# Kernel optimization log

Measured on AMD Instinct MI355X. Metric: run time of the kernel, lower is better.

## Reference

```python
import jax, jax.numpy as jnp
import numpy as np

WINDOW_SIZE = 11
SIGMA = 1.5
C1 = 0.0001
C2 = 0.0009


def _gaussian_kernel(window_size, channels):
    # 1D gaussian, sigma=1.5 (standard SSIM window), normalized
    ax = np.arange(window_size, dtype=np.float32) - (window_size - 1) / 2.0
    g = np.exp(-(ax ** 2) / (2.0 * SIGMA ** 2))
    g = g / g.sum()
    k2d = np.outer(g, g).astype(np.float32)  # [w, w], sums to 1
    # depthwise kernel, OIHW with groups=channels -> [C, 1, w, w]
    return jnp.asarray(np.tile(k2d[None, None], (channels, 1, 1, 1)))


def _dwconv(x, kernel):
    p = WINDOW_SIZE // 2
    return jax.lax.conv_general_dilated(
        x, kernel,
        window_strides=(1, 1),
        padding=[(p, p), (p, p)],
        dimension_numbers=('NCHW', 'OIHW', 'NCHW'),
        feature_group_count=x.shape[1],
    )


def setup_inputs() -> dict:
    key = jax.random.key(0)
    k1, k2 = jax.random.split(key)
    B, C, H, W = 16, 3, 512, 512
    x = jax.random.uniform(k1, (B, C, H, W), dtype=jnp.float32)
    y = jax.random.uniform(k2, (B, C, H, W), dtype=jnp.float32)
    return {"x": x, "y": y}


def reference(x, y):
    kernel = _gaussian_kernel(WINDOW_SIZE, x.shape[1])
    mean_sr = _dwconv(x, kernel)
    mean_hr = _dwconv(y, kernel)
    mean_sr_sq = mean_sr * mean_sr
    mean_hr_sq = mean_hr * mean_hr
    var_sr = _dwconv(x * x, kernel) - mean_sr_sq
    var_hr = _dwconv(y * y, kernel) - mean_hr_sq
    covar = _dwconv(x * y, kernel) - mean_sr * mean_hr
    ssim_pix = ((2.0 * mean_sr * mean_hr + C1) * (2.0 * covar + C2)
                / ((mean_sr_sq + mean_hr_sq + C1) * (var_sr + var_hr + C2)))
    ssim_mean = jnp.mean(ssim_pix)
    loss = -jnp.log10(ssim_mean)
    return (loss, ssim_mean)
```

## Files before the change

### kernel.cpp

```cpp
#include <hip/hip_runtime.h>
#include <hip/hip_fp16.h>
#include <math.h>

#define IMG    512
#define TWD    64
#define NSTRIP 2
#define BROWS  64
#define WIN    42
#define HS2    34
#define NBLK   3072
#define NPIX   12582912.0

constexpr float G[11] = {
    0.00102838f, 0.00759876f, 0.03600077f, 0.10936069f, 0.21300554f,
    0.26601173f,
    0.21300554f, 0.10936069f, 0.03600077f, 0.00759876f, 0.00102838f};

__device__ __forceinline__ void issue_loads(
    const float* __restrict__ px, const float* __restrict__ py, int gc0,
    float4 (&fx)[6], float4 (&fy)[6])
{
#pragma unroll
    for (int i = 0; i < 6; ++i) {
        int gcl = min(max(gc0 + 4 * i, 0), IMG - 4);
        fx[i] = *(const float4*)(px + gcl);
        fy[i] = *(const float4*)(py + gcl);
    }
}

__device__ __forceinline__ void conv_store(
    __half2 (&hb2)[4][WIN][HS2],
    const float4 (&fx)[6], const float4 (&fy)[6],
    int grow, int gc0, int bufrow, int hg)
{
    const float rm = ((unsigned)grow < IMG) ? 1.f : 0.f;
    float ax[8] = {}, ay[8] = {}, ass[8] = {}, axy[8] = {};
#pragma unroll
    for (int i = 0; i < 6; ++i) {
        const float gm = ((unsigned)(gc0 + 4 * i) < IMG) ? rm : 0.f;
        const float vx4[4] = {fx[i].x, fx[i].y, fx[i].z, fx[i].w};
        const float vy4[4] = {fy[i].x, fy[i].y, fy[i].z, fy[i].w};
#pragma unroll
        for (int c = 0; c < 4; ++c) {
            const int j = 4 * i + c;
            if (j < 3 || j > 20) continue;
            const float a  = vx4[c] * gm;
            const float b  = vy4[c] * gm;
            const float ss = fmaf(a, a, b * b);
            const float xy = a * b;
#pragma unroll
            for (int e = 0; e < 8; ++e) {
                const int k = j - 3 - e;
                if (k >= 0 && k <= 10) {
                    ax[e]  = fmaf(G[k], a,  ax[e]);
                    ay[e]  = fmaf(G[k], b,  ay[e]);
                    ass[e] = fmaf(G[k], ss, ass[e]);
                    axy[e] = fmaf(G[k], xy, axy[e]);
                }
            }
        }
    }
    const int p0 = 4 * hg;
#pragma unroll
    for (int p = 0; p < 4; ++p) {
        hb2[0][bufrow][p0 + p] = __floats2half2_rn(ax[2*p],  ax[2*p+1]);
        hb2[1][bufrow][p0 + p] = __floats2half2_rn(ay[2*p],  ay[2*p+1]);
        hb2[2][bufrow][p0 + p] = __floats2half2_rn(ass[2*p], ass[2*p+1]);
        hb2[3][bufrow][p0 + p] = __floats2half2_rn(axy[2*p], axy[2*p+1]);
    }
}

__device__ __forceinline__ float vpass16(
    const __half2 (&hb2)[4][WIN][HS2], const __half2 (&Gh)[11],
    int rb, int cg)
{
    __half2 vr[4][4];
    const __half2 z2 = __floats2half2_rn(0.f, 0.f);
#pragma unroll
    for (int q = 0; q < 4; ++q)
#pragma unroll
        for (int j = 0; j < 4; ++j) vr[q][j] = z2;
#pragma unroll
    for (int q = 0; q < 4; ++q)
#pragma unroll
        for (int k = 0; k < 14; ++k) {
            __half2 v = hb2[q][rb + k][cg];
#pragma unroll
            for (int j = 0; j < 4; ++j)
                if (k - j >= 0 && k - j <= 10)
                    vr[q][j] = __hfma2(Gh[k - j], v, vr[q][j]);
        }
    float s = 0.f;
#pragma unroll
    for (int j = 0; j < 4; ++j) {
        float2 mxv  = __half22float2(vr[0][j]);
        float2 myv  = __half22float2(vr[1][j]);
        float2 mssv = __half22float2(vr[2][j]);
        float2 mxyv = __half22float2(vr[3][j]);
        const float mxa[2]  = {mxv.x, mxv.y};
        const float mya[2]  = {myv.x, myv.y};
        const float mssa[2] = {mssv.x, mssv.y};
        const float mxya[2] = {mxyv.x, mxyv.y};
#pragma unroll
        for (int e = 0; e < 2; ++e) {
            float mx = mxa[e], my = mya[e];
            float mss = mssa[e], mxy = mxya[e];
            float mx2 = mx * mx, my2 = my * my, mxmy = mx * my;
            float num = (2.f * mxmy + 0.0001f) * (2.f * (mxy - mxmy) + 0.0009f);
            float den = (mx2 + my2 + 0.0001f) * ((mss - mx2 - my2) + 0.0009f);
            s += num * __builtin_amdgcn_rcpf(den);
        }
    }
    return s;
}

__global__ __launch_bounds__(256) void ssim_tile_kernel(
    const float* __restrict__ x, const float* __restrict__ y,
    float* __restrict__ partial)
{
    __shared__ __half2 hb2[4][WIN][HS2];
    __shared__ float wsum[4];

    const int tid = threadIdx.x;
    const int bx = blockIdx.x, by = blockIdx.y;
    const int c0 = bx * TWD;
    const int rbase0 = by * BROWS;
    const size_t ioff = (size_t)blockIdx.z * IMG * IMG;
    const float* __restrict__ xb = x + ioff;
    const float* __restrict__ yb = y + ioff;

    __half2 Gh[11];
#pragma unroll
    for (int k = 0; k < 11; ++k) Gh[k] = __floats2half2_rn(G[k], G[k]);

    const int hrow = tid >> 3;
    const int hg   = tid & 7;
    const int gc0  = c0 - 8 + 8 * hg;
    const int cg   = tid & 31;
    const int rb   = (tid >> 5) * 4;
    float lsum = 0.f;

    float4 pfx[6], pfy[6];

    {
        int brow = tid >> 3, g = tid & 7;
        int grow = rbase0 - 5 + brow;
        int tg0 = c0 - 8 + 8 * g;
        const float* px = xb + min(max(grow, 0), IMG - 1) * IMG;
        const float* py = yb + min(max(grow, 0), IMG - 1) * IMG;
        float4 fx[6], fy[6];
        issue_loads(px, py, tg0, fx, fy);
        conv_store(hb2, fx, fy, grow, tg0, brow, g);
    }
    if (tid < 80) {
        int t = tid + 256;
        int brow = t >> 3, g = t & 7;
        int grow = rbase0 - 5 + brow;
        int tg0 = c0 - 8 + 8 * g;
        const float* px = xb + min(max(grow, 0), IMG - 1) * IMG;
        const float* py = yb + min(max(grow, 0), IMG - 1) * IMG;
        float4 fx[6], fy[6];
        issue_loads(px, py, tg0, fx, fy);
        conv_store(hb2, fx, fy, grow, tg0, brow, g);
    }
    {
        int grow = rbase0 + 32 + 5 + hrow;
        const float* px = xb + min(max(grow, 0), IMG - 1) * IMG;
        const float* py = yb + min(max(grow, 0), IMG - 1) * IMG;
        issue_loads(px, py, gc0, pfx, pfy);
    }
    __syncthreads();
    lsum += vpass16(hb2, Gh, rb, cg);
    __syncthreads();

    for (int s = 1; s < NSTRIP; ++s) {
#pragma unroll
        for (int k = 0; k < 3; ++k) {
            int idx = tid + k * 256;
            if (idx < 640) {
                int q = idx / 160, rem = idx - q * 160;
                int rr = rem >> 4, p = rem & 15;
                *(float2*)&hb2[q][rr][2 * p] =
                    *(const float2*)&hb2[q][32 + rr][2 * p];
            }
        }
        __syncthreads();
        {
            int grow = rbase0 + 32 * s + 5 + hrow;
            conv_store(hb2, pfx, pfy, grow, gc0, 10 + hrow, hg);
        }
        if (s < NSTRIP - 1) {
            int grow = rbase0 + 32 * (s + 1) + 5 + hrow;
            const float* px = xb + min(max(grow, 0), IMG - 1) * IMG;
            const float* py = yb + min(max(grow, 0), IMG - 1) * IMG;
            issue_loads(px, py, gc0, pfx, pfy);
        }
        __syncthreads();
        lsum += vpass16(hb2, Gh, rb, cg);
        __syncthreads();
    }

#pragma unroll
    for (int off = 32; off > 0; off >>= 1)
        lsum += __shfl_down(lsum, off, 64);
    if ((tid & 63) == 0) wsum[tid >> 6] = lsum;
    __syncthreads();
    if (tid == 0) {
        float ssum = wsum[0] + wsum[1] + wsum[2] + wsum[3];
        int bid = bx + 8 * (by + 8 * blockIdx.z);
        partial[bid] = ssum;
    }
}

__global__ __launch_bounds__(1024) void ssim_reduce_kernel(
    const float* __restrict__ partial, float* __restrict__ out)
{
    __shared__ double ws[16];
    const int tid = threadIdx.x;
    double s = 0.0;
#pragma unroll
    for (int i = 0; i < NBLK / 1024; ++i) s += (double)partial[tid + i * 1024];
#pragma unroll
    for (int off = 32; off > 0; off >>= 1)
        s += __shfl_down(s, off, 64);
    if ((tid & 63) == 0) ws[tid >> 6] = s;
    __syncthreads();
    if (tid == 0) {
        double t = 0.0;
#pragma unroll
        for (int w = 0; w < 16; ++w) t += ws[w];
        double mean = t / NPIX;
        out[0] = (float)(-log10(mean));
        out[1] = (float)mean;
    }
}

extern "C" void kernel_launch(void* const* d_in, const int* in_sizes, int n_in,
                              void* d_out, int out_size, void* d_ws, size_t ws_size,
                              hipStream_t stream)
{
    const float* x = (const float*)d_in[0];
    const float* y = (const float*)d_in[1];
    float* out     = (float*)d_out;
    float* partial = (float*)d_ws;

    dim3 grid(8, 8, 48);
    ssim_tile_kernel<<<grid, 256, 0, stream>>>(x, y, partial);
    ssim_reduce_kernel<<<1, 1024, 0, stream>>>(partial, out);
}
```

Before: 52.53 us.

## Use single-strip 32-row tiles, XCD-aware block remap, unmasked interior path

Drops the two-strip sliding window with its register prefetch and LDS row shift. Each block now handles one 32-row strip, so twice as many blocks are launched and each does a full 42-row horizontal pass. Block IDs are remapped so consecutive hardware block IDs, which spread across XCDs, cover contiguous image regions. Interior tiles skip clamping and masking via a templated fast path. In exchange, halo rows are recomputed more often (42 per 32 output rows instead of 74 per 64), which adds global load and horizontal-pass work.

```diff
diff --git a/kernel.cpp b/kernel.cpp
--- a/kernel.cpp
+++ b/kernel.cpp
@@ -2,50 +2,46 @@
 #include <hip/hip_fp16.h>
 #include <math.h>
 
-#define IMG    512
-#define TWD    64
-#define NSTRIP 2
-#define BROWS  64
-#define WIN    42
-#define HS2    34
-#define NBLK   3072
-#define NPIX   12582912.0
+#define IMG   512
+#define TWD   64
+#define BROWS 32
+#define WIN   42
+#define HS2   34
+#define NBLK  6144
+#define NPIX  12582912.0
 
 constexpr float G[11] = {
     0.00102838f, 0.00759876f, 0.03600077f, 0.10936069f, 0.21300554f,
     0.26601173f,
     0.21300554f, 0.10936069f, 0.03600077f, 0.00759876f, 0.00102838f};
 
-__device__ __forceinline__ void issue_loads(
-    const float* __restrict__ px, const float* __restrict__ py, int gc0,
-    float4 (&fx)[6], float4 (&fy)[6])
-{
-#pragma unroll
-    for (int i = 0; i < 6; ++i) {
-        int gcl = min(max(gc0 + 4 * i, 0), IMG - 4);
-        fx[i] = *(const float4*)(px + gcl);
-        fy[i] = *(const float4*)(py + gcl);
-    }
-}
-
+template<bool MASKED>
 __device__ __forceinline__ void conv_store(
     __half2 (&hb2)[4][WIN][HS2],
     const float4 (&fx)[6], const float4 (&fy)[6],
     int grow, int gc0, int bufrow, int hg)
 {
-    const float rm = ((unsigned)grow < IMG) ? 1.f : 0.f;
+    float gm[6];
+#pragma unroll
+    for (int i = 0; i < 6; ++i) {
+        if (MASKED) {
+            const float rm = ((unsigned)grow < IMG) ? 1.f : 0.f;
+            gm[i] = ((unsigned)(gc0 + 4 * i) < IMG) ? rm : 0.f;
+        } else {
+            gm[i] = 1.f;
+        }
+    }
     float ax[8] = {}, ay[8] = {}, ass[8] = {}, axy[8] = {};
 #pragma unroll
     for (int i = 0; i < 6; ++i) {
-        const float gm = ((unsigned)(gc0 + 4 * i) < IMG) ? rm : 0.f;
         const float vx4[4] = {fx[i].x, fx[i].y, fx[i].z, fx[i].w};
         const float vy4[4] = {fy[i].x, fy[i].y, fy[i].z, fy[i].w};
 #pragma unroll
         for (int c = 0; c < 4; ++c) {
             const int j = 4 * i + c;
             if (j < 3 || j > 20) continue;
-            const float a  = vx4[c] * gm;
-            const float b  = vy4[c] * gm;
+            const float a  = MASKED ? vx4[c] * gm[i] : vx4[c];
+            const float b  = MASKED ? vy4[c] * gm[i] : vy4[c];
             const float ss = fmaf(a, a, b * b);
             const float xy = a * b;
 #pragma unroll
@@ -70,6 +66,37 @@
     }
 }
 
+template<bool MASKED>
+__device__ __forceinline__ void htask(
+    __half2 (&hb2)[4][WIN][HS2],
+    const float* __restrict__ xb, const float* __restrict__ yb,
+    int rbase0, int c0, int t)
+{
+    const int brow = t >> 3, g = t & 7;
+    const int grow = rbase0 - 5 + brow;
+    const int gc0  = c0 - 8 + 8 * g;
+    float4 fx[6], fy[6];
+    if (MASKED) {
+        const float* __restrict__ px = xb + min(max(grow, 0), IMG - 1) * IMG;
+        const float* __restrict__ py = yb + min(max(grow, 0), IMG - 1) * IMG;
+#pragma unroll
+        for (int i = 0; i < 6; ++i) {
+            int gcl = min(max(gc0 + 4 * i, 0), IMG - 4);
+            fx[i] = *(const float4*)(px + gcl);
+            fy[i] = *(const float4*)(py + gcl);
+        }
+    } else {
+        const float* __restrict__ px = xb + grow * IMG + gc0;
+        const float* __restrict__ py = yb + grow * IMG + gc0;
+#pragma unroll
+        for (int i = 0; i < 6; ++i) {
+            fx[i] = *(const float4*)(px + 4 * i);
+            fy[i] = *(const float4*)(py + 4 * i);
+        }
+    }
+    conv_store<MASKED>(hb2, fx, fy, grow, gc0, brow, g);
+}
+
 __device__ __forceinline__ float vpass16(
     const __half2 (&hb2)[4][WIN][HS2], const __half2 (&Gh)[11],
     int rb, int cg)
@@ -122,94 +149,43 @@
     __shared__ float wsum[4];
 
     const int tid = threadIdx.x;
-    const int bx = blockIdx.x, by = blockIdx.y;
+    const int bid = blockIdx.x;
+    const int nb  = (bid & 7) * (NBLK / 8) + (bid >> 3);
+    const int z   = nb >> 7;
+    const int rem = nb & 127;
+    const int by  = rem >> 3, bx = rem & 7;
     const int c0 = bx * TWD;
     const int rbase0 = by * BROWS;
-    const size_t ioff = (size_t)blockIdx.z * IMG * IMG;
+    const size_t ioff = (size_t)z * IMG * IMG;
     const float* __restrict__ xb = x + ioff;
     const float* __restrict__ yb = y + ioff;
 
+    const bool interior = (bx >= 1) & (bx <= 6) & (by >= 1) & (by <= 14);
+
     __half2 Gh[11];
 #pragma unroll
     for (int k = 0; k < 11; ++k) Gh[k] = __floats2half2_rn(G[k], G[k]);
 
-    const int hrow = tid >> 3;
-    const int hg   = tid & 7;
-    const int gc0  = c0 - 8 + 8 * hg;
-    const int cg   = tid & 31;
-    const int rb   = (tid >> 5) * 4;
-    float lsum = 0.f;
-
-    float4 pfx[6], pfy[6];
-
-    {
-        int brow = tid >> 3, g = tid & 7;
-        int grow = rbase0 - 5 + brow;
-        int tg0 = c0 - 8 + 8 * g;
-        const float* px = xb + min(max(grow, 0), IMG - 1) * IMG;
-        const float* py = yb + min(max(grow, 0), IMG - 1) * IMG;
-        float4 fx[6], fy[6];
-        issue_loads(px, py, tg0, fx, fy);
-        conv_store(hb2, fx, fy, grow, tg0, brow, g);
-    }
-    if (tid < 80) {
-        int t = tid + 256;
-        int brow = t >> 3, g = t & 7;
-        int grow = rbase0 - 5 + brow;
-        int tg0 = c0 - 8 + 8 * g;
-        const float* px = xb + min(max(grow, 0), IMG - 1) * IMG;
-        const float* py = yb + min(max(grow, 0), IMG - 1) * IMG;
-        float4 fx[6], fy[6];
-        issue_loads(px, py, tg0, fx, fy);
-        conv_store(hb2, fx, fy, grow, tg0, brow, g);
-    }
-    {
-        int grow = rbase0 + 32 + 5 + hrow;
-        const float* px = xb + min(max(grow, 0), IMG - 1) * IMG;
-        const float* py = yb + min(max(grow, 0), IMG - 1) * IMG;
-        issue_loads(px, py, gc0, pfx, pfy);
+    if (interior) {
+        htask<false>(hb2, xb, yb, rbase0, c0, tid);
+        if (tid < 80) htask<false>(hb2, xb, yb, rbase0, c0, tid + 256);
+    } else {
+        htask<true>(hb2, xb, yb, rbase0, c0, tid);
+        if (tid < 80) htask<true>(hb2, xb, yb, rbase0, c0, tid + 256);
     }
     __syncthreads();
-    lsum += vpass16(hb2, Gh, rb, cg);
-    __syncthreads();
-
-    for (int s = 1; s < NSTRIP; ++s) {
-#pragma unroll
-        for (int k = 0; k < 3; ++k) {
-            int idx = tid + k * 256;
-            if (idx < 640) {
-                int q = idx / 160, rem = idx - q * 160;
-                int rr = rem >> 4, p = rem & 15;
-                *(float2*)&hb2[q][rr][2 * p] =
-                    *(const float2*)&hb2[q][32 + rr][2 * p];
-            }
-        }
-        __syncthreads();
-        {
-            int grow = rbase0 + 32 * s + 5 + hrow;
-            conv_store(hb2, pfx, pfy, grow, gc0, 10 + hrow, hg);
-        }
-        if (s < NSTRIP - 1) {
-            int grow = rbase0 + 32 * (s + 1) + 5 + hrow;
-            const float* px = xb + min(max(grow, 0), IMG - 1) * IMG;
-            const float* py = yb + min(max(grow, 0), IMG - 1) * IMG;
-            issue_loads(px, py, gc0, pfx, pfy);
-        }
-        __syncthreads();
-        lsum += vpass16(hb2, Gh, rb, cg);
-        __syncthreads();
-    }
+
+    const int cg = tid & 31;
+    const int rb = (tid >> 5) * 4;
+    float lsum = vpass16(hb2, Gh, rb, cg);
 
 #pragma unroll
     for (int off = 32; off > 0; off >>= 1)
         lsum += __shfl_down(lsum, off, 64);
     if ((tid & 63) == 0) wsum[tid >> 6] = lsum;
     __syncthreads();
-    if (tid == 0) {
-        float ssum = wsum[0] + wsum[1] + wsum[2] + wsum[3];
-        int bid = bx + 8 * (by + 8 * blockIdx.z);
-        partial[bid] = ssum;
-    }
+    if (tid == 0)
+        partial[bid] = wsum[0] + wsum[1] + wsum[2] + wsum[3];
 }
 
 __global__ __launch_bounds__(1024) void ssim_reduce_kernel(
@@ -244,7 +220,6 @@
     float* out     = (float*)d_out;
     float* partial = (float*)d_ws;
 
-    dim3 grid(8, 8, 48);
-    ssim_tile_kernel<<<grid, 256, 0, stream>>>(x, y, partial);
+    ssim_tile_kernel<<<NBLK, 256, 0, stream>>>(x, y, partial);
     ssim_reduce_kernel<<<1, 1024, 0, stream>>>(partial, out);
 }
```

Measured after the change: 55.21 us. 5.1% more time.
